# Performance work log

Hardware: AMD Instinct MI355X
Metric: run time of the kernel (lower is better)

The kernel has to match this reference:

```python
import jax, jax.numpy as jnp
import numpy as np

D_STATE = 16
D_CONV = 4


def _ln_cf(x, w, b, eps=1e-6):
    # channels_first LayerNorm over dim 1 of (B,C,H,W)
    u = x.mean(1, keepdims=True)
    s = ((x - u) ** 2).mean(1, keepdims=True)
    return w[:, None, None] * ((x - u) / jnp.sqrt(s + eps)) + b[:, None, None]


def _ln_last(x, w, b, eps=1e-5):
    u = x.mean(-1, keepdims=True)
    s = ((x - u) ** 2).mean(-1, keepdims=True)
    return (x - u) / jnp.sqrt(s + eps) * w + b


def _mamba(xn, Win, convw, convb, Wx, Wdt, bdt, Alog, Dp):
    # xn: (B, L, d_model); returns (B, L, d_inner) (out_proj is Identity in this module)
    B, L, _ = xn.shape
    di = Win.shape[0] // 2
    xz = xn @ Win.T                                   # (B,L,2*di), in_proj bias=False
    xc, z = xz[..., :di], xz[..., di:]
    # causal depthwise conv1d along L (pad left d_conv-1, slice == torch pad+trim)
    xt = jnp.pad(xc.transpose(0, 2, 1), ((0, 0), (0, 0), (D_CONV - 1, 0)))
    xt = jax.lax.conv_general_dilated(xt, convw[:, None, :], (1,), 'VALID',
                                      dimension_numbers=('NCH', 'OIH', 'NCH'),
                                      feature_group_count=di)
    xs = jax.nn.silu(xt + convb[None, :, None]).transpose(0, 2, 1)  # (B,L,di)
    dtr = Wdt.shape[1]
    x_dbl = xs @ Wx.T                                 # (B,L,dtr+2*ds)
    dt = x_dbl[..., :dtr]
    Bm = x_dbl[..., dtr:dtr + D_STATE]                # (B,L,ds)
    Cm = x_dbl[..., dtr + D_STATE:]                   # (B,L,ds)
    delta = jax.nn.softplus(dt @ Wdt.T + bdt)         # (B,L,di)
    A = -jnp.exp(Alog)                                # (di,ds)
    dA = jnp.exp(delta[..., None] * A)                # (B,L,di,ds)
    dBx = delta[..., None] * Bm[:, :, None, :] * xs[..., None]

    def step(h, ab):
        a, b2 = ab
        h = a * h + b2
        return h, h

    h0 = jnp.zeros((B, di, D_STATE), xn.dtype)
    _, hs = jax.lax.scan(step, h0, (dA.transpose(1, 0, 2, 3), dBx.transpose(1, 0, 2, 3)))
    y = jnp.einsum('lbds,bls->bld', hs, Cm) + xs * Dp
    return y * jax.nn.silu(z)


def _dwconv2d(u, k, dil):
    c = k.shape[0]
    return jax.lax.conv_general_dilated(u, k[:, None], (1, 1),
                                        [(dil, dil), (dil, dil)],
                                        rhs_dilation=(dil, dil),
                                        dimension_numbers=('NCHW', 'OIHW', 'NCHW'),
                                        feature_group_count=c)


def _block(x, gamma1, gamma2, ln1_w, ln1_b, mn_w, mn_b,
           f_Win, f_convw, f_convb, f_Wx, f_Wdt, f_bdt, f_Alog, f_D,
           b_Win, b_convw, b_convb, b_Wx, b_Wdt, b_bdt, b_Alog, b_D,
           Wout, msff_win, msff_dw1, msff_dw2, msff_dw3, msff_wout):
    B, C, H, W = x.shape
    L = H * W
    # --- BiPixelMambaLayer branch ---
    x1 = _ln_cf(x, ln1_w, ln1_b)                       # norm1 (channels_first)
    xf = x1.reshape(B, C, L).transpose(0, 2, 1)        # (B,L,C)
    xn = _ln_last(xf, mn_w, mn_b)                      # inner nn.LayerNorm (eps=1e-5)
    yf = _mamba(xn, f_Win, f_convw, f_convb, f_Wx, f_Wdt, f_bdt, f_Alog, f_D)
    yb = _mamba(xn[:, ::-1], b_Win, b_convw, b_convb, b_Wx, b_Wdt, b_bdt, b_Alog, b_D)
    yo = (yf + yb[:, ::-1]) @ Wout.T                   # shared out_proj (bias=False)
    x = x + gamma1[:, None, None] * (yo.transpose(0, 2, 1).reshape(B, C, H, W) + x1)
    # --- MSFF branch (norm1 reused) ---
    inp = x
    xm = _ln_cf(x, ln1_w, ln1_b)
    h = jnp.einsum('oc,bchw->bohw', msff_win, xm)      # project_in (1x1x1 conv, depth=1)
    hid = msff_dw1.shape[0]
    h1 = _dwconv2d(h[:, :hid], msff_dw1, 1)            # Conv3d 3x3x3 w/ depth=1 == 2D center slice
    h2 = _dwconv2d(h[:, hid:2 * hid], msff_dw2, 2)
    h3 = _dwconv2d(h[:, 2 * hid:], msff_dw3, 3)
    g = jax.nn.gelu(h1, approximate=False) * h2 * h3
    xm = jnp.einsum('oc,bchw->bohw', msff_wout, g)     # project_out
    return inp + gamma2[:, None, None] * xm


def setup_inputs() -> dict:
    key = jax.random.key(0)
    ks = jax.random.split(key, 40)
    dim, di, dtr, ds, hid, Bn, H, W = 96, 192, 6, 16, 192, 2, 64, 64
    r = lambda i, shape, s=0.05: jax.random.normal(ks[i], shape, jnp.float32) * s
    inp = {
        'x': r(0, (Bn, dim, H, W), 1.0),
        'gamma1': r(1, (dim,), 0.1), 'gamma2': r(2, (dim,), 0.1),
        'ln1_w': 1.0 + r(3, (dim,), 0.1), 'ln1_b': r(4, (dim,), 0.1),
        'mn_w': 1.0 + r(5, (dim,), 0.1), 'mn_b': r(6, (dim,), 0.1),
    }
    i = 7
    for p in ('f_', 'b_'):
        inp[p + 'Win'] = r(i, (2 * di, dim)); i += 1
        inp[p + 'convw'] = r(i, (di, D_CONV), 0.2); i += 1
        inp[p + 'convb'] = r(i, (di,), 0.1); i += 1
        inp[p + 'Wx'] = r(i, (dtr + 2 * ds, di)); i += 1
        inp[p + 'Wdt'] = r(i, (di, dtr), 0.1); i += 1
        inp[p + 'bdt'] = r(i, (di,), 0.1); i += 1
        inp[p + 'Alog'] = jax.random.uniform(ks[i], (di, ds), jnp.float32, 0.0, 2.5); i += 1
        inp[p + 'D'] = r(i, (di,), 0.5); i += 1
    inp['Wout'] = r(i, (dim, di)); i += 1
    inp['msff_win'] = r(i, (3 * hid, dim)); i += 1
    inp['msff_dw1'] = r(i, (hid, 3, 3), 0.2); i += 1
    inp['msff_dw2'] = r(i, (hid, 3, 3), 0.2); i += 1
    inp['msff_dw3'] = r(i, (hid, 3, 3), 0.2); i += 1
    inp['msff_wout'] = r(i, (dim, hid)); i += 1
    return inp


def reference(x, gamma1, gamma2, ln1_w, ln1_b, mn_w, mn_b,
              f_Win, f_convw, f_convb, f_Wx, f_Wdt, f_bdt, f_Alog, f_D,
              b_Win, b_convw, b_convb, b_Wx, b_Wdt, b_bdt, b_Alog, b_D,
              Wout, msff_win, msff_dw1, msff_dw2, msff_dw3, msff_wout):
    return _block(x, gamma1, gamma2, ln1_w, ln1_b, mn_w, mn_b,
                  f_Win, f_convw, f_convb, f_Wx, f_Wdt, f_bdt, f_Alog, f_D,
                  b_Win, b_convw, b_convb, b_Wx, b_Wdt, b_bdt, b_Alog, b_D,
                  Wout, msff_win, msff_dw1, msff_dw2, msff_dw3, msff_wout)
```

## Files before the change

kernel.cpp:

```cpp
#include <hip/hip_runtime.h>
#include <hip/hip_bf16.h>
#include <math.h>

typedef __hip_bfloat16 bf16;
typedef _Float16 f16;
typedef f16  f16x8  __attribute__((ext_vector_type(8)));
typedef short short8 __attribute__((ext_vector_type(8)));
typedef unsigned short ushort8 __attribute__((ext_vector_type(8)));
typedef float floatx4 __attribute__((ext_vector_type(4)));

#define L_SEQ 4096
#define BATCH 2
#define DIM   96
#define DI    192
#define DS    16
#define HID   192
#define NPOS  (BATCH * L_SEQ)
#define NCH   1024
#define CHUNK 4
#define NREC  (2 * BATCH * DI)
#define LDBL  40
#define LOG2E 1.44269504088896f
#define TP    32

__device__ __forceinline__ float silu_f(float x) { return x / (1.f + __expf(-x)); }
__device__ __forceinline__ float softplus_f(float x) {
    return fmaxf(x, 0.f) + __logf(1.f + __expf(-fabsf(x)));
}
__device__ __forceinline__ float b2f(bf16 v) { return __bfloat162float(v); }
__device__ __forceinline__ float us2f(unsigned short u) {
    union { unsigned int i; float f; } cv; cv.i = ((unsigned int)u) << 16; return cv.f;
}

__global__ void k_prep(const float* __restrict__ fWin, const float* __restrict__ bWin,
                       const float* __restrict__ fWx,  const float* __restrict__ bWx,
                       const float* __restrict__ Wout, const float* __restrict__ mwin,
                       const float* __restrict__ mwout,
                       const float* __restrict__ fAlog, const float* __restrict__ bAlog,
                       const float* __restrict__ mdw1, const float* __restrict__ mdw2,
                       const float* __restrict__ mdw3,
                       bf16* __restrict__ war, float* __restrict__ a2tab,
                       float* __restrict__ mdwt) {
    int i = blockIdx.x * blockDim.x + threadIdx.x;
    if (i < 180480) {
        float v;
        if (i < 36864)        v = fWin[i];
        else if (i < 73728)   v = bWin[i - 36864];
        else if (i < 81024)   v = fWx[i - 73728];
        else if (i < 88320)   v = bWx[i - 81024];
        else if (i < 106752)  v = Wout[i - 88320];
        else if (i < 162048)  v = mwin[i - 106752];
        else                  v = mwout[i - 162048];
        war[i] = __float2bfloat16(v);
    } else if (i < 186624) {
        int j = i - 180480;
        int dir = j / 3072, rem = j % 3072;
        const float* al = dir ? bAlog : fAlog;
        a2tab[j] = -__expf(al[rem]) * LOG2E;
    } else if (i < 191808) {
        int j = i - 186624;
        int cv = j / 1728, rem = j % 1728;
        int tap = rem / 192, c = rem % 192;
        const float* src = (cv == 0) ? mdw1 : (cv == 1) ? mdw2 : mdw3;
        mdwt[j] = src[c * 9 + tap];
    }
}

__global__ void k_ln12_t(const float* __restrict__ x,
                         const float* __restrict__ ln1w, const float* __restrict__ ln1b,
                         const float* __restrict__ mnw,  const float* __restrict__ mnb,
                         float* __restrict__ X1, bf16* __restrict__ XNbf) {
    __shared__ float xt[DIM][TP + 1];
    __shared__ float rs[8][TP], rss[8][TP];
    __shared__ float uu[TP], rr[TP];
    int p0 = blockIdx.x * TP;
    int b = p0 >> 12, l0 = p0 & (L_SEQ - 1);
    int t = threadIdx.x;
    int tg = t >> 5, li = t & 31;

    for (int idx = t; idx < DIM * TP; idx += 256) {
        int c = idx >> 5, q = idx & 31;
        xt[c][q] = x[((size_t)(b * DIM + c)) * L_SEQ + l0 + q];
    }
    __syncthreads();
    {
        float s = 0.f, ss = 0.f;
        for (int c = tg; c < DIM; c += 8) { float v = xt[c][li]; s += v; ss += v * v; }
        rs[tg][li] = s; rss[tg][li] = ss;
    }
    __syncthreads();
    if (t < TP) {
        float s = 0.f, ss = 0.f;
#pragma unroll
        for (int g = 0; g < 8; g++) { s += rs[g][t]; ss += rss[g][t]; }
        float u = s / DIM;
        uu[t] = u; rr[t] = rsqrtf(ss / DIM - u * u + 1e-6f);
    }
    __syncthreads();
    {
        float u = uu[li], r = rr[li];
        float s2 = 0.f, ss2 = 0.f;
        for (int c = tg; c < DIM; c += 8) {
            float tv = ln1w[c] * (xt[c][li] - u) * r + ln1b[c];
            X1[((size_t)(b * DIM + c)) * L_SEQ + l0 + li] = tv;
            xt[c][li] = tv;
            s2 += tv; ss2 += tv * tv;
        }
        rs[tg][li] = s2; rss[tg][li] = ss2;
    }
    __syncthreads();
    if (t < TP) {
        float s = 0.f, ss = 0.f;
#pragma unroll
        for (int g = 0; g < 8; g++) { s += rs[g][t]; ss += rss[g][t]; }
        float u = s / DIM;
        uu[t] = u; rr[t] = rsqrtf(ss / DIM - u * u + 1e-5f);
    }
    __syncthreads();
    for (int idx = t; idx < DIM * TP; idx += 256) {
        int q = idx / DIM, c = idx % DIM;
        XNbf[(size_t)(p0 + q) * DIM + c] =
            __float2bfloat16((xt[c][q] - uu[q]) * rr[q] * mnw[c] + mnb[c]);
    }
}

__global__ void mfma_nt_dir(const bf16* __restrict__ A0, const bf16* __restrict__ A1,
                            const bf16* __restrict__ W0, const bf16* __restrict__ W1,
                            void* __restrict__ C0, void* __restrict__ C1,
                            int M, int N, int K, int ldc, int pad6, int obf) {
    int z = blockIdx.z;
    const bf16* A = z ? A1 : A0;
    const bf16* W = z ? W1 : W0;
    void* C = z ? C1 : C0;
    int wave = threadIdx.x >> 6, lane = threadIdx.x & 63;
    int m0 = blockIdx.x * 64 + wave * 16;
    int n0 = blockIdx.y * 64;
    int lm = lane & 15, quad = lane >> 4;
    const short* Ap = (const short*)A + (size_t)(m0 + lm) * K + quad * 8;
    const short* Wp = (const short*)W;
    floatx4 acc[4];
#pragma unroll
    for (int t = 0; t < 4; t++) acc[t] = (floatx4){0.f, 0.f, 0.f, 0.f};
    for (int k0 = 0; k0 < K; k0 += 32) {
        short8 a = *(const short8*)(Ap + k0);
#pragma unroll
        for (int t = 0; t < 4; t++) {
            int n = n0 + t * 16 + lm;
            short8 b = (n < N) ? *(const short8*)(Wp + (size_t)n * K + k0 + quad * 8)
                               : (short8){0,0,0,0,0,0,0,0};
            acc[t] = __builtin_amdgcn_mfma_f32_16x16x32_bf16(a, b, acc[t], 0, 0, 0);
        }
    }
#pragma unroll
    for (int t = 0; t < 4; t++) {
        int n = n0 + t * 16 + lm;
        if (n < N) {
            int nn = (pad6 && n >= 6) ? n + 2 : n;
#pragma unroll
            for (int r = 0; r < 4; r++) {
                int m = m0 + quad * 4 + r;
                if (obf) ((bf16*)C)[(size_t)m * ldc + nn] = __float2bfloat16(acc[t][r]);
                else     ((float*)C)[(size_t)m * ldc + nn] = acc[t][r];
            }
        }
    }
}

__global__ void mfma_nt(const bf16* __restrict__ A, const bf16* __restrict__ W,
                        bf16* __restrict__ C, int M, int N, int K, int ldc) {
    int wave = threadIdx.x >> 6, lane = threadIdx.x & 63;
    int m0 = blockIdx.x * 64 + wave * 16;
    int n0 = blockIdx.y * 64;
    int lm = lane & 15, quad = lane >> 4;
    const short* Ap = (const short*)A + (size_t)(m0 + lm) * K + quad * 8;
    const short* Wp = (const short*)W;
    floatx4 acc[4];
#pragma unroll
    for (int t = 0; t < 4; t++) acc[t] = (floatx4){0.f, 0.f, 0.f, 0.f};
    for (int k0 = 0; k0 < K; k0 += 32) {
        short8 a = *(const short8*)(Ap + k0);
#pragma unroll
        for (int t = 0; t < 4; t++) {
            int n = n0 + t * 16 + lm;
            short8 b = (n < N) ? *(const short8*)(Wp + (size_t)n * K + k0 + quad * 8)
                               : (short8){0,0,0,0,0,0,0,0};
            acc[t] = __builtin_amdgcn_mfma_f32_16x16x32_bf16(a, b, acc[t], 0, 0, 0);
        }
    }
#pragma unroll
    for (int t = 0; t < 4; t++) {
        int n = n0 + t * 16 + lm;
        if (n < N) {
#pragma unroll
            for (int r = 0; r < 4; r++) {
                int m = m0 + quad * 4 + r;
                C[(size_t)m * ldc + n] = __float2bfloat16(acc[t][r]);
            }
        }
    }
}

__global__ void mfma_out(const bf16* __restrict__ Y1, const bf16* __restrict__ Y2,
                         const bf16* __restrict__ W, float* __restrict__ C,
                         int M, int N, int K, int ldc) {
    int wave = threadIdx.x >> 6, lane = threadIdx.x & 63;
    int m0 = blockIdx.x * 64 + wave * 16;
    int n0 = blockIdx.y * 64;
    int lm = lane & 15, quad = lane >> 4;
    const short* A1p = (const short*)Y1 + (size_t)(m0 + lm) * K + quad * 8;
    const short* A2p = (const short*)Y2 + (size_t)(m0 + lm) * K + quad * 8;
    const short* Wp  = (const short*)W;
    floatx4 acc[4];
#pragma unroll
    for (int t = 0; t < 4; t++) acc[t] = (floatx4){0.f, 0.f, 0.f, 0.f};
    for (int k0 = 0; k0 < K; k0 += 32) {
        short8 a1 = *(const short8*)(A1p + k0);
        short8 a2 = *(const short8*)(A2p + k0);
#pragma unroll
        for (int t = 0; t < 4; t++) {
            int n = n0 + t * 16 + lm;
            short8 b = (n < N) ? *(const short8*)(Wp + (size_t)n * K + k0 + quad * 8)
                               : (short8){0,0,0,0,0,0,0,0};
            acc[t] = __builtin_amdgcn_mfma_f32_16x16x32_bf16(a1, b, acc[t], 0, 0, 0);
            acc[t] = __builtin_amdgcn_mfma_f32_16x16x32_bf16(a2, b, acc[t], 0, 0, 0);
        }
    }
#pragma unroll
    for (int t = 0; t < 4; t++) {
        int n = n0 + t * 16 + lm;
        if (n < N) {
#pragma unroll
            for (int r = 0; r < 4; r++) {
                int m = m0 + quad * 4 + r;
                C[(size_t)m * ldc + n] = acc[t][r];
            }
        }
    }
}

__global__ void mfma_msffout(const bf16* __restrict__ A, const bf16* __restrict__ Bm,
                             const float* __restrict__ XMID, const float* __restrict__ gamma2,
                             float* __restrict__ out, int M, int K) {
    int wave = threadIdx.x >> 6, lane = threadIdx.x & 63;
    int m0 = blockIdx.x * 64 + wave * 16;
    int n0 = blockIdx.y * 64;
    int lm = lane & 15, quad = lane >> 4;
    int am = m0 + lm;
    bool aval = am < M;
    const short* Ap = (const short*)A + (size_t)am * K + quad * 8;
    const short* Bp = (const short*)Bm;
    floatx4 acc[4];
#pragma unroll
    for (int t = 0; t < 4; t++) acc[t] = (floatx4){0.f, 0.f, 0.f, 0.f};
    for (int k0 = 0; k0 < K; k0 += 32) {
        short8 a = aval ? *(const short8*)(Ap + k0) : (short8){0,0,0,0,0,0,0,0};
#pragma unroll
        for (int t = 0; t < 4; t++) {
            int n = n0 + t * 16 + lm;
            short8 b = *(const short8*)(Bp + (size_t)n * K + k0 + quad * 8);
            acc[t] = __builtin_amdgcn_mfma_f32_16x16x32_bf16(a, b, acc[t], 0, 0, 0);
        }
    }
#pragma unroll
    for (int t = 0; t < 4; t++) {
        int n = n0 + t * 16 + lm;
        int b = n >> 12, l = n & (L_SEQ - 1);
#pragma unroll
        for (int r = 0; r < 4; r++) {
            int m = m0 + quad * 4 + r;
            if (m < M) {
                size_t idx = ((size_t)(b * M + m)) * L_SEQ + l;
                out[idx] = XMID[idx] + gamma2[m] * acc[t][r];
            }
        }
    }
}

__global__ void k_conv_v(const bf16* __restrict__ XZF, const bf16* __restrict__ XZB,
                         const float* __restrict__ fw, const float* __restrict__ fb,
                         const float* __restrict__ bw, const float* __restrict__ bb,
                         bf16* __restrict__ XSF, bf16* __restrict__ XSB) {
    int dirb = blockIdx.y;
    int i = blockIdx.x * blockDim.x + threadIdx.x;
    int dg = i % 24;
    int p = i / 24;
    int b = p >> 12, l = p & (L_SEQ - 1);
    int d0 = dg * 8;
    const bf16* XZ = dirb ? XZB : XZF;
    const float* cw = dirb ? bw : fw;
    const float* cb = dirb ? bb : fb;

    float4 w[8];
#pragma unroll
    for (int j = 0; j < 8; j++) w[j] = *(const float4*)(cw + (d0 + j) * 4);
    float acc[8];
#pragma unroll
    for (int j = 0; j < 8; j++) acc[j] = cb[d0 + j];

#pragma unroll
    for (int k = 0; k < 4; k++) {
        int ls = dirb ? (l + 3 - k) : (l - 3 + k);
        if (ls >= 0 && ls < L_SEQ) {
            ushort8 xv = *(const ushort8*)((const unsigned short*)XZ +
                           ((size_t)(b * L_SEQ + ls)) * 384 + d0);
#pragma unroll
            for (int j = 0; j < 8; j++) {
                float wk = (k == 0) ? w[j].x : (k == 1) ? w[j].y : (k == 2) ? w[j].z : w[j].w;
                acc[j] += wk * us2f(xv[j]);
            }
        }
    }
    ushort8 ov;
#pragma unroll
    for (int j = 0; j < 8; j++) {
        bf16 t = __float2bfloat16(silu_f(acc[j]));
        ov[j] = *(unsigned short*)&t;
    }
    *(ushort8*)((unsigned short*)(dirb ? XSB : XSF) + (size_t)p * DI + d0) = ov;
}

__global__ void k_scan_p1(const float* __restrict__ DBLF, const float* __restrict__ DBLB,
                          const bf16* __restrict__ XSF,  const bf16* __restrict__ XSB,
                          const float* __restrict__ fWdt, const float* __restrict__ fbdt,
                          const float* __restrict__ bWdt, const float* __restrict__ bbdt,
                          const float* __restrict__ a2tab,
                          f16* __restrict__ P, f16* __restrict__ Q) {
    int t = blockIdx.x * blockDim.x + threadIdx.x;
    int d = t % DI;
    int g = t / DI;
    int chunk = g & (NCH - 1);
    int dirb = g >> 10;
    int b = dirb & 1, dir = dirb >> 1;

    const float* DBL = dir ? DBLB : DBLF;
    const bf16*  XS  = dir ? XSB  : XSF;
    const float* wdt = (dir ? bWdt : fWdt) + d * 6;
    float bdtv = (dir ? bbdt : fbdt)[d];

    float wd[6];
#pragma unroll
    for (int r = 0; r < 6; r++) wd[r] = wdt[r];
    const float* a2p = a2tab + (dir * DI + d) * 16;
    float A2[16], h[16];
#pragma unroll
    for (int v = 0; v < 4; v++) {
        float4 a2v = *(const float4*)(a2p + 4 * v);
        A2[4*v] = a2v.x; A2[4*v+1] = a2v.y; A2[4*v+2] = a2v.z; A2[4*v+3] = a2v.w;
    }
#pragma unroll
    for (int s = 0; s < 16; s++) h[s] = 0.f;

    int l = dir ? (L_SEQ - 1 - chunk * CHUNK) : chunk * CHUNK;
    int stp = dir ? -1 : 1;
    float sumdel = 0.f;

#pragma unroll
    for (int i = 0; i < CHUNK; i++) {
        size_t p = (size_t)b * L_SEQ + l;
        const float* row = DBL + p * LDBL;
        float dtv = bdtv;
#pragma unroll
        for (int r = 0; r < 6; r++) dtv += row[r] * wd[r];
        float del = softplus_f(dtv);
        float xs  = b2f(XS[p * DI + d]);
        const float4* bm = (const float4*)(row + 8);
        float4 B0 = bm[0], B1 = bm[1], B2 = bm[2], B3 = bm[3];
        float Bm[16] = {B0.x,B0.y,B0.z,B0.w, B1.x,B1.y,B1.z,B1.w,
                        B2.x,B2.y,B2.z,B2.w, B3.x,B3.y,B3.z,B3.w};
        float dx = del * xs;
        sumdel += del;
#pragma unroll
        for (int s = 0; s < 16; s++) {
            float dA = exp2f(del * A2[s]);
            h[s] = dA * h[s] + dx * Bm[s];
        }
        l += stp;
    }
    size_t idx = ((size_t)g * DI + d) * 16;
    f16x8 q0, q1, p0, p1;
#pragma unroll
    for (int j = 0; j < 8; j++) {
        q0[j] = (f16)h[j];
        q1[j] = (f16)h[8 + j];
        p0[j] = (f16)exp2f(A2[j] * sumdel);
        p1[j] = (f16)exp2f(A2[8 + j] * sumdel);
    }
    *(f16x8*)(Q + idx)     = q0;
    *(f16x8*)(Q + idx + 8) = q1;
    *(f16x8*)(P + idx)     = p0;
    *(f16x8*)(P + idx + 8) = p1;
}

__global__ void k_scan_p2(const f16* __restrict__ P, f16* __restrict__ Q) {
    int u = blockIdx.x * blockDim.x + threadIdx.x;
    int s = u & 15;
    int dd = (u >> 4) % DI;
    int dirb = u / (DI * 16);
    float run = 0.f;
#pragma unroll 8
    for (int c = 0; c < NCH; c++) {
        size_t i = (((size_t)(dirb * NCH + c)) * DI + dd) * 16 + s;
        float tmp = (float)Q[i];
        Q[i] = (f16)run;
        run = (float)P[i] * run + tmp;
    }
}

__global__ void k_scan_p3(const float* __restrict__ DBLF, const float* __restrict__ DBLB,
                          const bf16* __restrict__ XSF,  const bf16* __restrict__ XSB,
                          const bf16* __restrict__ XZF,  const bf16* __restrict__ XZB,
                          const float* __restrict__ fWdt, const float* __restrict__ fbdt,
                          const float* __restrict__ bWdt, const float* __restrict__ bbdt,
                          const float* __restrict__ a2tab,
                          const float* __restrict__ fD,    const float* __restrict__ bD,
                          const f16* __restrict__ Q,
                          bf16* __restrict__ YSF, bf16* __restrict__ YSB) {
    int t = blockIdx.x * blockDim.x + threadIdx.x;
    int d = t % DI;
    int g = t / DI;
    int chunk = g & (NCH - 1);
    int dirb = g >> 10;
    int b = dirb & 1, dir = dirb >> 1;

    const float* DBL = dir ? DBLB : DBLF;
    const bf16*  XS  = dir ? XSB  : XSF;
    const bf16*  XZ  = dir ? XZB  : XZF;
    const float* wdt = (dir ? bWdt : fWdt) + d * 6;
    float bdtv = (dir ? bbdt : fbdt)[d];
    float Dp = dir ? bD[d] : fD[d];
    bf16* Y = dir ? YSB : YSF;

    float wd[6];
#pragma unroll
    for (int r = 0; r < 6; r++) wd[r] = wdt[r];
    const float* a2p = a2tab + (dir * DI + d) * 16;
    float A2[16], h[16];
#pragma unroll
    for (int v = 0; v < 4; v++) {
        float4 a2v = *(const float4*)(a2p + 4 * v);
        A2[4*v] = a2v.x; A2[4*v+1] = a2v.y; A2[4*v+2] = a2v.z; A2[4*v+3] = a2v.w;
    }
    size_t idx = ((size_t)g * DI + d) * 16;
    f16x8 q0 = *(const f16x8*)(Q + idx);
    f16x8 q1 = *(const f16x8*)(Q + idx + 8);
#pragma unroll
    for (int j = 0; j < 8; j++) { h[j] = (float)q0[j]; h[8 + j] = (float)q1[j]; }

    int l = dir ? (L_SEQ - 1 - chunk * CHUNK) : chunk * CHUNK;
    int stp = dir ? -1 : 1;

#pragma unroll
    for (int i = 0; i < CHUNK; i++) {
        size_t p = (size_t)b * L_SEQ + l;
        const float* row = DBL + p * LDBL;
        float dtv = bdtv;
#pragma unroll
        for (int r = 0; r < 6; r++) dtv += row[r] * wd[r];
        float del = softplus_f(dtv);
        float xs  = b2f(XS[p * DI + d]);
        float z   = b2f(XZ[p * 384 + 192 + d]);
        const float4* bm = (const float4*)(row + 8);
        float4 B0 = bm[0], B1 = bm[1], B2 = bm[2], B3 = bm[3];
        float4 C0 = bm[4], C1 = bm[5], C2 = bm[6], C3 = bm[7];
        float Bm[16] = {B0.x,B0.y,B0.z,B0.w, B1.x,B1.y,B1.z,B1.w,
                        B2.x,B2.y,B2.z,B2.w, B3.x,B3.y,B3.z,B3.w};
        float Cm[16] = {C0.x,C0.y,C0.z,C0.w, C1.x,C1.y,C1.z,C1.w,
                        C2.x,C2.y,C2.z,C2.w, C3.x,C3.y,C3.z,C3.w};
        float dx = del * xs;
        float pr = 0.f;
#pragma unroll
        for (int s = 0; s < 16; s++) {
            float dA = exp2f(del * A2[s]);
            h[s] = dA * h[s] + dx * Bm[s];
            pr += h[s] * Cm[s];
        }
        Y[p * DI + d] = __float2bfloat16((pr + xs * Dp) * silu_f(z));
        l += stp;
    }
}

__global__ void k_mid_t(const float* __restrict__ x, const float* __restrict__ YO,
                        const float* __restrict__ X1,
                        const float* __restrict__ gamma1,
                        const float* __restrict__ ln1w, const float* __restrict__ ln1b,
                        float* __restrict__ XMID, bf16* __restrict__ XM2cl) {
    __shared__ float vt[DIM][TP + 1];
    __shared__ float yt[DIM][TP + 1];
    __shared__ float rs[8][TP], rss[8][TP];
    __shared__ float uu[TP], rr[TP];
    int p0 = blockIdx.x * TP;
    int b = p0 >> 12, l0 = p0 & (L_SEQ - 1);
    int t = threadIdx.x;
    int tg = t >> 5, li = t & 31;

    for (int idx = t; idx < DIM * TP; idx += 256) {
        int q = idx / DIM, c = idx % DIM;
        yt[c][q] = YO[(size_t)(p0 + q) * DIM + c];
    }
    __syncthreads();
    {
        float s = 0.f, ss = 0.f;
        for (int c = tg; c < DIM; c += 8) {
            size_t gi = ((size_t)(b * DIM + c)) * L_SEQ + l0 + li;
            float v = x[gi] + gamma1[c] * (yt[c][li] + X1[gi]);
            XMID[gi] = v;
            vt[c][li] = v;
            s += v; ss += v * v;
        }
        rs[tg][li] = s; rss[tg][li] = ss;
    }
    __syncthreads();
    if (t < TP) {
        float s = 0.f, ss = 0.f;
#pragma unroll
        for (int g = 0; g < 8; g++) { s += rs[g][t]; ss += rss[g][t]; }
        float u = s / DIM;
        uu[t] = u; rr[t] = rsqrtf(ss / DIM - u * u + 1e-6f);
    }
    __syncthreads();
    for (int idx = t; idx < DIM * TP; idx += 256) {
        int q = idx / DIM, c = idx % DIM;
        XM2cl[(size_t)(p0 + q) * DIM + c] =
            __float2bfloat16(ln1w[c] * (vt[c][q] - uu[q]) * rr[q] + ln1b[c]);
    }
}

__global__ void k_msff_v(const bf16* __restrict__ H, const float* __restrict__ mdwt,
                         bf16* __restrict__ G) {
    int i = blockIdx.x * blockDim.x + threadIdx.x;
    int cg = i % 24;
    int p = i / 24;
    int c0 = cg * 8;
    int b = p >> 12, l = p & (L_SEQ - 1);
    int y = l >> 6, xc = l & 63;
    float a1[8] = {}, a2[8] = {}, a3[8] = {};
    const unsigned short* Hu = (const unsigned short*)H;

#pragma unroll
    for (int ky = 0; ky < 3; ky++) {
#pragma unroll
        for (int kx = 0; kx < 3; kx++) {
            int tap = ky * 3 + kx;
            {
                int y1 = y + (ky - 1), x1 = xc + (kx - 1);
                if (y1 >= 0 && y1 < 64 && x1 >= 0 && x1 < 64) {
                    float4 w0 = *(const float4*)(mdwt + tap * 192 + c0);
                    float4 w1 = *(const float4*)(mdwt + tap * 192 + c0 + 4);
                    ushort8 hv = *(const ushort8*)(Hu +
                        ((size_t)(b * L_SEQ + y1 * 64 + x1)) * 576 + c0);
                    float wv[8] = {w0.x,w0.y,w0.z,w0.w, w1.x,w1.y,w1.z,w1.w};
#pragma unroll
                    for (int j = 0; j < 8; j++) a1[j] += wv[j] * us2f(hv[j]);
                }
            }
            {
                int y2 = y + (ky - 1) * 2, x2 = xc + (kx - 1) * 2;
                if (y2 >= 0 && y2 < 64 && x2 >= 0 && x2 < 64) {
                    float4 w0 = *(const float4*)(mdwt + (9 + tap) * 192 + c0);
                    float4 w1 = *(const float4*)(mdwt + (9 + tap) * 192 + c0 + 4);
                    ushort8 hv = *(const ushort8*)(Hu +
                        ((size_t)(b * L_SEQ + y2 * 64 + x2)) * 576 + 192 + c0);
                    float wv[8] = {w0.x,w0.y,w0.z,w0.w, w1.x,w1.y,w1.z,w1.w};
#pragma unroll
                    for (int j = 0; j < 8; j++) a2[j] += wv[j] * us2f(hv[j]);
                }
            }
            {
                int y3 = y + (ky - 1) * 3, x3 = xc + (kx - 1) * 3;
                if (y3 >= 0 && y3 < 64 && x3 >= 0 && x3 < 64) {
                    float4 w0 = *(const float4*)(mdwt + (18 + tap) * 192 + c0);
                    float4 w1 = *(const float4*)(mdwt + (18 + tap) * 192 + c0 + 4);
                    ushort8 hv = *(const ushort8*)(Hu +
                        ((size_t)(b * L_SEQ + y3 * 64 + x3)) * 576 + 384 + c0);
                    float wv[8] = {w0.x,w0.y,w0.z,w0.w, w1.x,w1.y,w1.z,w1.w};
#pragma unroll
                    for (int j = 0; j < 8; j++) a3[j] += wv[j] * us2f(hv[j]);
                }
            }
        }
    }
    ushort8 ov;
#pragma unroll
    for (int j = 0; j < 8; j++) {
        float ge = 0.5f * a1[j] * (1.f + erff(a1[j] * 0.70710678118f));
        bf16 t = __float2bfloat16(ge * a2[j] * a3[j]);
        ov[j] = *(unsigned short*)&t;
    }
    *(ushort8*)((unsigned short*)G + (size_t)p * HID + c0) = ov;
}

extern "C" void kernel_launch(void* const* d_in, const int* in_sizes, int n_in,
                              void* d_out, int out_size, void* d_ws, size_t ws_size,
                              hipStream_t stream) {
    const float* x      = (const float*)d_in[0];
    const float* gamma1 = (const float*)d_in[1];
    const float* gamma2 = (const float*)d_in[2];
    const float* ln1w   = (const float*)d_in[3];
    const float* ln1b   = (const float*)d_in[4];
    const float* mnw    = (const float*)d_in[5];
    const float* mnb    = (const float*)d_in[6];
    const float* fWin   = (const float*)d_in[7];
    const float* fconvw = (const float*)d_in[8];
    const float* fconvb = (const float*)d_in[9];
    const float* fWx    = (const float*)d_in[10];
    const float* fWdt   = (const float*)d_in[11];
    const float* fbdt   = (const float*)d_in[12];
    const float* fAlog  = (const float*)d_in[13];
    const float* fD     = (const float*)d_in[14];
    const float* bWin   = (const float*)d_in[15];
    const float* bconvw = (const float*)d_in[16];
    const float* bconvb = (const float*)d_in[17];
    const float* bWx    = (const float*)d_in[18];
    const float* bWdt   = (const float*)d_in[19];
    const float* bbdt   = (const float*)d_in[20];
    const float* bAlog  = (const float*)d_in[21];
    const float* bD     = (const float*)d_in[22];
    const float* Wout   = (const float*)d_in[23];
    const float* mwin   = (const float*)d_in[24];
    const float* mdw1   = (const float*)d_in[25];
    const float* mdw2   = (const float*)d_in[26];
    const float* mdw3   = (const float*)d_in[27];
    const float* mwout  = (const float*)d_in[28];
    float* out = (float*)d_out;

    float* ws = (float*)d_ws;
    float* X1    = ws;
    bf16*  XNbf  = (bf16*)(ws + 786432);
    bf16*  XZF   = (bf16*)(ws + 1179648);
    bf16*  XZB   = (bf16*)(ws + 2752512);
    bf16*  XSF   = (bf16*)(ws + 4325376);
    bf16*  XSB   = (bf16*)(ws + 5111808);
    float* DBLF  = ws + 5898240;
    float* DBLB  = ws + 6225920;
    f16*   Ph    = (f16*)(ws + 6553600);
    f16*   Qh    = (f16*)(ws + 12845056);
    bf16*  YSFbf = (bf16*)(ws + 19136512);
    bf16*  YSBbf = (bf16*)(ws + 19922944);
    float* YO    = ws + 20709376;
    float* XMID  = ws + 21495808;
    bf16*  XM2cl = (bf16*)(ws + 22282240);
    bf16*  Hcl   = (bf16*)(ws + 22675456);
    bf16*  Gcl   = (bf16*)(ws + 25034752);
    bf16*  WAR   = (bf16*)(ws + 25821184);
    float* A2tab = ws + 25911424;
    float* MDWT  = ws + 25917568;

    const bf16* fWinB  = WAR;
    const bf16* bWinB  = WAR + 36864;
    const bf16* fWxB   = WAR + 73728;
    const bf16* bWxB   = WAR + 81024;
    const bf16* WoutB  = WAR + 88320;
    const bf16* mwinB  = WAR + 106752;
    const bf16* mwoutB = WAR + 162048;

    k_prep<<<750, 256, 0, stream>>>(fWin, bWin, fWx, bWx, Wout, mwin, mwout,
                                    fAlog, bAlog, mdw1, mdw2, mdw3,
                                    WAR, A2tab, MDWT);
    k_ln12_t<<<NPOS / TP, 256, 0, stream>>>(x, ln1w, ln1b, mnw, mnb, X1, XNbf);
    mfma_nt_dir<<<dim3(128, 6, 2), 256, 0, stream>>>(XNbf, XNbf, fWinB, bWinB,
                                                     XZF, XZB, NPOS, 384, DIM, 384, 0, 1);
    k_conv_v<<<dim3(NPOS * 24 / 256, 2), 256, 0, stream>>>(XZF, XZB, fconvw, fconvb,
                                                           bconvw, bconvb, XSF, XSB);
    mfma_nt_dir<<<dim3(128, 1, 2), 256, 0, stream>>>(XSF, XSB, fWxB, bWxB,
                                                     DBLF, DBLB, NPOS, 38, DI, LDBL, 1, 0);
    k_scan_p1<<<NREC * NCH / 256, 256, 0, stream>>>(DBLF, DBLB, XSF, XSB,
                                                    fWdt, fbdt, bWdt, bbdt,
                                                    A2tab, Ph, Qh);
    k_scan_p2<<<NREC * 16 / 256, 256, 0, stream>>>(Ph, Qh);
    k_scan_p3<<<NREC * NCH / 256, 256, 0, stream>>>(DBLF, DBLB, XSF, XSB, XZF, XZB,
                                                    fWdt, fbdt, bWdt, bbdt,
                                                    A2tab, fD, bD, Qh,
                                                    YSFbf, YSBbf);
    mfma_out<<<dim3(128, 2), 256, 0, stream>>>(YSFbf, YSBbf, WoutB, YO, NPOS, DIM, DI, DIM);
    k_mid_t<<<NPOS / TP, 256, 0, stream>>>(x, YO, X1, gamma1, ln1w, ln1b, XMID, XM2cl);
    mfma_nt<<<dim3(128, 9), 256, 0, stream>>>(XM2cl, mwinB, Hcl, NPOS, 576, DIM, 576);
    k_msff_v<<<NPOS * 24 / 256, 256, 0, stream>>>(Hcl, MDWT, Gcl);
    mfma_msffout<<<dim3(2, 128), 256, 0, stream>>>(mwoutB, Gcl, XMID, gamma2, out, DIM, HID);
}
```

Before: 315.8 us.

## Split chunk-carry scan into hierarchical three-pass group scan

Replaces the single serial carry-propagation kernel, which looped over all 1024 chunks per state lane, with a three-level scan. Chunks are reduced in groups of 32 into fp32 group products and offsets, a short scan runs over the 32 groups, and each group is then rescanned to write the per-chunk carries. This is meant to remove the long serial dependency chain and the low thread count of the old pass. The cost is two extra launches, extra workspace, and a second read of P and Q.

```diff
diff --git a/kernel.cpp b/kernel.cpp
--- a/kernel.cpp
+++ b/kernel.cpp
@@ -18,6 +18,8 @@
 #define NPOS  (BATCH * L_SEQ)
 #define NCH   1024
 #define CHUNK 4
+#define GRP   32
+#define NGRP  (NCH / GRP)
 #define NREC  (2 * BATCH * DI)
 #define LDBL  40
 #define LOG2E 1.44269504088896f
@@ -391,18 +393,84 @@
     *(f16x8*)(P + idx + 8) = p1;
 }
 
-__global__ void k_scan_p2(const f16* __restrict__ P, f16* __restrict__ Q) {
+__global__ void k_scan_p2a(const f16* __restrict__ P, const f16* __restrict__ Q,
+                           float* __restrict__ Pg, float* __restrict__ Qg) {
+    int t = blockIdx.x * blockDim.x + threadIdx.x;
+    int s8 = t & 1;
+    int d = (t >> 1) % DI;
+    int rest = t / (DI * 2);
+    int grp = rest % NGRP;
+    int dirb = rest / NGRP;
+
+    float Pr[8], Qr[8];
+#pragma unroll
+    for (int j = 0; j < 8; j++) { Pr[j] = 1.f; Qr[j] = 0.f; }
+
+    size_t base = (((size_t)(dirb * NCH + grp * GRP)) * DI + d) * 16 + s8 * 8;
+    for (int i = 0; i < GRP; i++) {
+        size_t idx = base + (size_t)i * (DI * 16);
+        f16x8 p8 = *(const f16x8*)(P + idx);
+        f16x8 q8 = *(const f16x8*)(Q + idx);
+#pragma unroll
+        for (int j = 0; j < 8; j++) {
+            float pv = (float)p8[j], qv = (float)q8[j];
+            Qr[j] = pv * Qr[j] + qv;
+            Pr[j] *= pv;
+        }
+    }
+    size_t gidx = (((size_t)(dirb * NGRP + grp)) * DI + d) * 16 + s8 * 8;
+#pragma unroll
+    for (int v = 0; v < 2; v++) {
+        *(float4*)(Pg + gidx + 4 * v) = make_float4(Pr[4*v], Pr[4*v+1], Pr[4*v+2], Pr[4*v+3]);
+        *(float4*)(Qg + gidx + 4 * v) = make_float4(Qr[4*v], Qr[4*v+1], Qr[4*v+2], Qr[4*v+3]);
+    }
+}
+
+__global__ void k_scan_p2b(const float* __restrict__ Pg, float* __restrict__ Qg) {
     int u = blockIdx.x * blockDim.x + threadIdx.x;
     int s = u & 15;
     int dd = (u >> 4) % DI;
     int dirb = u / (DI * 16);
-    float run = 0.f;
-#pragma unroll 8
-    for (int c = 0; c < NCH; c++) {
-        size_t i = (((size_t)(dirb * NCH + c)) * DI + dd) * 16 + s;
-        float tmp = (float)Q[i];
-        Q[i] = (f16)run;
-        run = (float)P[i] * run + tmp;
+    float runP = 1.f, runQ = 0.f;
+#pragma unroll
+    for (int g = 0; g < NGRP; g++) {
+        size_t i = (((size_t)(dirb * NGRP + g)) * DI + dd) * 16 + s;
+        float pg = Pg[i], qg = Qg[i];
+        Qg[i] = runQ;
+        runQ = pg * runQ + qg;
+        runP *= pg;
+    }
+}
+
+__global__ void k_scan_p2c(const f16* __restrict__ P, f16* __restrict__ Q,
+                           const float* __restrict__ Qg) {
+    int t = blockIdx.x * blockDim.x + threadIdx.x;
+    int s8 = t & 1;
+    int d = (t >> 1) % DI;
+    int rest = t / (DI * 2);
+    int grp = rest % NGRP;
+    int dirb = rest / NGRP;
+
+    size_t gidx = (((size_t)(dirb * NGRP + grp)) * DI + d) * 16 + s8 * 8;
+    float runQ[8];
+#pragma unroll
+    for (int v = 0; v < 2; v++) {
+        float4 qv = *(const float4*)(Qg + gidx + 4 * v);
+        runQ[4*v] = qv.x; runQ[4*v+1] = qv.y; runQ[4*v+2] = qv.z; runQ[4*v+3] = qv.w;
+    }
+
+    size_t base = (((size_t)(dirb * NCH + grp * GRP)) * DI + d) * 16 + s8 * 8;
+    for (int i = 0; i < GRP; i++) {
+        size_t idx = base + (size_t)i * (DI * 16);
+        f16x8 p8 = *(const f16x8*)(P + idx);
+        f16x8 q8 = *(const f16x8*)(Q + idx);
+        f16x8 o8;
+#pragma unroll
+        for (int j = 0; j < 8; j++) {
+            o8[j] = (f16)runQ[j];
+            runQ[j] = (float)p8[j] * runQ[j] + (float)q8[j];
+        }
+        *(f16x8*)(Q + idx) = o8;
     }
 }
 
@@ -644,6 +712,8 @@
     bf16*  WAR   = (bf16*)(ws + 25821184);
     float* A2tab = ws + 25911424;
     float* MDWT  = ws + 25917568;
+    float* Pgb   = ws + 25922752;
+    float* Qgb   = ws + 26315968;
 
     const bf16* fWinB  = WAR;
     const bf16* bWinB  = WAR + 36864;
@@ -666,7 +736,9 @@
     k_scan_p1<<<NREC * NCH / 256, 256, 0, stream>>>(DBLF, DBLB, XSF, XSB,
                                                     fWdt, fbdt, bWdt, bbdt,
                                                     A2tab, Ph, Qh);
-    k_scan_p2<<<NREC * 16 / 256, 256, 0, stream>>>(Ph, Qh);
+    k_scan_p2a<<<4 * NGRP * DI * 2 / 256, 256, 0, stream>>>(Ph, Qh, Pgb, Qgb);
+    k_scan_p2b<<<NREC * 16 / 256, 256, 0, stream>>>(Pgb, Qgb);
+    k_scan_p2c<<<4 * NGRP * DI * 2 / 256, 256, 0, stream>>>(Ph, Qh, Qgb);
     k_scan_p3<<<NREC * NCH / 256, 256, 0, stream>>>(DBLF, DBLB, XSF, XSB, XZF, XZB,
                                                     fWdt, fbdt, bWdt, bbdt,
                                                     A2tab, fD, bD, Qh,
```

After: 290.0 us. -8.2%, faster.
